# Performance work log

Hardware: AMD Instinct MI355X
Metric: run time of the kernel (lower is better)

The kernel has to match this reference:

```python
import jax, jax.numpy as jnp
import numpy as np

NUM_USERS = 600000
NUM_ITEMS = 400000
NUM_NODES = NUM_USERS + NUM_ITEMS
DIM = 64
NUM_EDGES = 8000000


def setup_inputs() -> dict:
    key = jax.random.key(0)
    k1, k2, k3, k4 = jax.random.split(key, 4)
    users_emb = jax.random.normal(k1, (NUM_USERS, DIM), dtype=jnp.float32)
    items_emb = jax.random.normal(k2, (NUM_ITEMS, DIM), dtype=jnp.float32)
    edge_index = jax.random.randint(k3, (2, NUM_EDGES), 0, NUM_NODES, dtype=jnp.int64)
    edge_values = jax.random.uniform(k4, (NUM_EDGES,), dtype=jnp.float32)
    return {
        "users_emb": users_emb,
        "items_emb": items_emb,
        "edge_index": edge_index,
        "edge_values": edge_values,
    }


def reference(users_emb, items_emb, edge_index, edge_values):
    # all_emb = cat([users_emb, items_emb])  -> [N, d]
    num_user = users_emb.shape[0]
    num_item = items_emb.shape[0]
    all_emb = jnp.concatenate([users_emb, items_emb], axis=0)
    # SpMM: out[r] = sum_{e: row[e]==r} val[e] * all_emb[col[e]]
    rows, cols = edge_index[0], edge_index[1]
    messages = all_emb[cols] * edge_values[:, None]  # [E, d] gather + scale
    out = jax.ops.segment_sum(messages, rows, num_segments=num_user + num_item)
    h_u2 = out[:num_user]
    h_i2 = out[num_user:]
    return (h_u2, h_i2)
```

## Files before the change

kernel.cpp:

```cpp
#include <hip/hip_runtime.h>

#define DIM 64
#define RPB 1024
#define RPB_SHIFT 10
#define NBMAX 1024
#define CHUNK 4096
#define EPT 16
#define CAPT 35
#define SREC_CAP (CAPT * 256)
#define NPGF 32

typedef unsigned long long u64;
typedef unsigned int u32;
typedef unsigned short u16;
typedef float f4v __attribute__((ext_vector_type(4)));
typedef _Float16 h4 __attribute__((ext_vector_type(4)));
typedef _Float16 h8 __attribute__((ext_vector_type(8)));

__global__ void detect_idx_width(const unsigned int* __restrict__ idx_words,
                                 int* __restrict__ flag) {
    __shared__ unsigned int s_or[256];
    unsigned int acc = 0;
    for (int i = threadIdx.x; i < 4096; i += blockDim.x)
        acc |= idx_words[2 * i + 1];
    s_or[threadIdx.x] = acc;
    __syncthreads();
    for (int s = 128; s > 0; s >>= 1) {
        if (threadIdx.x < s) s_or[threadIdx.x] |= s_or[threadIdx.x + s];
        __syncthreads();
    }
    if (threadIdx.x == 0) *flag = (s_or[0] == 0) ? 1 : 0;
}

__device__ __forceinline__ int load_idx(const void* ei, int use64, long long i) {
    return use64 ? (int)((const long long*)ei)[i] : ((const int*)ei)[i];
}

__device__ __forceinline__ int load_idx_nt(const void* ei, int use64, long long i) {
    return use64 ? (int)__builtin_nontemporal_load(&((const long long*)ei)[i])
                 : __builtin_nontemporal_load(&((const int*)ei)[i]);
}

__device__ __forceinline__ u32 quad_scan_ex(u32 qs, u32* wtot, int tid, u32* total_out) {
    u32 inc = qs;
    #pragma unroll
    for (int d = 1; d < 64; d <<= 1) {
        u32 v = __shfl_up(inc, d, 64);
        if ((tid & 63) >= d) inc += v;
    }
    if ((tid & 63) == 63) wtot[tid >> 6] = inc;
    __syncthreads();
    int w = tid >> 6;
    u32 woff = 0;
    #pragma unroll
    for (int k = 0; k < 3; ++k) woff += (k < w) ? wtot[k] : 0;
    if (total_out) *total_out = wtot[0] + wtot[1] + wtot[2] + wtot[3];
    return woff + inc - qs;
}

__global__ __launch_bounds__(256) void convert_emb(const f4v* __restrict__ u4,
                                                   const f4v* __restrict__ i4,
                                                   long long usz4, long long tot4,
                                                   h4* __restrict__ dst) {
    long long stride = (long long)gridDim.x * blockDim.x;
    for (long long idx = (long long)blockIdx.x * blockDim.x + threadIdx.x;
         idx < tot4; idx += stride) {
        const f4v* src = (idx < usz4) ? (u4 + idx) : (i4 + (idx - usz4));
        f4v f = __builtin_nontemporal_load(src);
        h4 o;
        o.x = (_Float16)f.x; o.y = (_Float16)f.y;
        o.z = (_Float16)f.z; o.w = (_Float16)f.w;
        dst[idx] = o;
    }
}

__global__ __launch_bounds__(256) void hist_coarse(const void* __restrict__ ei,
                                                   const int* __restrict__ flag,
                                                   int* __restrict__ counts,
                                                   int num_edges) {
    __shared__ int h[NBMAX];
    for (int b = threadIdx.x; b < NBMAX; b += 256) h[b] = 0;
    __syncthreads();
    int use64 = *flag;
    long long tid = (long long)blockIdx.x * 256 + threadIdx.x;
    long long stride = (long long)gridDim.x * 256;
    long long npairs = (long long)num_edges >> 1;
    const u64* p = (const u64*)ei;
    if (use64) {
        for (long long e = tid; e < npairs; e += stride) {
            u64 a = __builtin_nontemporal_load(&p[2 * e]);
            u64 b = __builtin_nontemporal_load(&p[2 * e + 1]);
            atomicAdd(&h[(int)(u32)a >> RPB_SHIFT], 1);
            atomicAdd(&h[(int)(u32)b >> RPB_SHIFT], 1);
        }
    } else {
        for (long long e = tid; e < npairs; e += stride) {
            u64 v = __builtin_nontemporal_load(&p[e]);
            atomicAdd(&h[(int)(u32)v >> RPB_SHIFT], 1);
            atomicAdd(&h[(int)(u32)(v >> 32) >> RPB_SHIFT], 1);
        }
    }
    if (tid == 0 && (num_edges & 1)) {
        int r = load_idx(ei, use64, num_edges - 1);
        atomicAdd(&h[r >> RPB_SHIFT], 1);
    }
    __syncthreads();
    for (int b = threadIdx.x; b < NBMAX; b += 256)
        if (h[b]) atomicAdd(&counts[b], h[b]);
}

__global__ __launch_bounds__(256) void scan_buckets(const int* __restrict__ counts,
                                                    int* __restrict__ offs,
                                                    int* __restrict__ gcursor,
                                                    int* __restrict__ offs2, int nbkt) {
    __shared__ u32 wtot[4];
    int t = threadIdx.x;
    int4 h = ((const int4*)counts)[t];
    u32 qs = (u32)(h.x + h.y + h.z + h.w);
    u32 total;
    u32 ex = quad_scan_ex(qs, wtot, t, &total);
    int o0 = (int)ex, o1 = o0 + h.x, o2 = o1 + h.y, o3 = o2 + h.z;
    offs[4*t] = o0; offs[4*t+1] = o1; offs[4*t+2] = o2; offs[4*t+3] = o3;
    gcursor[4*t] = o0; gcursor[4*t+1] = o1; gcursor[4*t+2] = o2; gcursor[4*t+3] = o3;
    if (t == 255) {
        offs[NBMAX] = (int)total;
        if (offs2) offs2[(long long)nbkt << RPB_SHIFT] = (int)total;
    }
}

__global__ __launch_bounds__(256) void bin_edges(const void* __restrict__ ei,
                                                 const float* __restrict__ vals,
                                                 const int* __restrict__ flag,
                                                 int* __restrict__ gcursor,
                                                 u64* __restrict__ recs,
                                                 int num_edges) {
    __shared__ u32 hist[NBMAX];
    __shared__ u32 scanL[NBMAX];
    __shared__ u32 gbase[NBMAX];
    __shared__ u32 wtot[4];
    __shared__ u64 payload[CHUNK];
    __shared__ u16 bidv[CHUNK];

    int tid = threadIdx.x;
    long long base = (long long)blockIdx.x * CHUNK;
    int n = (int)min((long long)CHUNK, (long long)num_edges - base);
    int use64 = *flag;

    for (int b = tid; b < NBMAX; b += 256) hist[b] = 0;
    __syncthreads();

    int rows_[EPT]; int cols_[EPT]; float ws_[EPT];
    #pragma unroll
    for (int i = 0; i < EPT; ++i) {
        int j = tid + i * 256;
        rows_[i] = -1;
        if (j < n) {
            long long e = base + j;
            rows_[i] = load_idx_nt(ei, use64, e);
            cols_[i] = load_idx_nt(ei, use64, (long long)num_edges + e);
            ws_[i]   = __builtin_nontemporal_load(&vals[e]);
            atomicAdd(&hist[rows_[i] >> RPB_SHIFT], 1u);
        }
    }
    __syncthreads();

    u32 h0 = hist[4*tid], h1 = hist[4*tid+1], h2 = hist[4*tid+2], h3 = hist[4*tid+3];
    u32 ex = quad_scan_ex(h0 + h1 + h2 + h3, wtot, tid, nullptr);
    scanL[4*tid]   = ex;
    scanL[4*tid+1] = ex + h0;
    scanL[4*tid+2] = ex + h0 + h1;
    scanL[4*tid+3] = ex + h0 + h1 + h2;
    __syncthreads();

    for (int b = tid; b < NBMAX; b += 256) {
        u32 c = hist[b];
        gbase[b] = c ? (u32)atomicAdd(&gcursor[b], (int)c) : 0u;
    }
    __syncthreads();
    for (int b = tid; b < NBMAX; b += 256) hist[b] = scanL[b];
    __syncthreads();

    #pragma unroll
    for (int i = 0; i < EPT; ++i) {
        if (rows_[i] >= 0) {
            int b = rows_[i] >> RPB_SHIFT;
            u32 pos = atomicAdd(&hist[b], 1u);
            u32 rl = (u32)(rows_[i] & (RPB - 1));
            payload[pos] = ((u64)__float_as_uint(ws_[i]) << 32) | (rl << 20) | (u32)cols_[i];
            bidv[pos] = (u16)b;
        }
    }
    __syncthreads();

    for (int j = tid; j < n; j += 256) {
        u64 rec = payload[j];
        int b = bidv[j];
        recs[gbase[b] + (u32)j - scanL[b]] = rec;
    }
}

#define ACC8(P0, P1, W, V) \
    P0.x += W * (float)V[0]; P0.y += W * (float)V[1]; \
    P0.z += W * (float)V[2]; P0.w += W * (float)V[3]; \
    P1.x += W * (float)V[4]; P1.y += W * (float)V[5]; \
    P1.z += W * (float)V[6]; P1.w += W * (float)V[7];

__global__ __launch_bounds__(256, 2) void sortgather_h(const int* __restrict__ offs,
                                                       const u64* __restrict__ recs,
                                                       const h8* __restrict__ hemb8,
                                                       float* __restrict__ out,
                                                       int num_nodes) {
    __shared__ u64 s_recs[SREC_CAP];
    __shared__ u32 node_beg[RPB + 1];
    __shared__ u32 cursor[RPB];
    __shared__ u32 wtot[4];

    int b  = blockIdx.x;
    int t  = threadIdx.x;
    int l8 = t & 7;
    int g  = t >> 3;
    int beg = offs[b], end = offs[b + 1];
    int cnt = end - beg;
    int row0 = b << RPB_SHIFT;

    if (cnt <= SREC_CAP) {
        u64 r_[CAPT];
        #pragma unroll
        for (int k = 0; k < CAPT; ++k) {
            int j = t + k * 256;
            r_[k] = (j < cnt) ? __builtin_nontemporal_load(&recs[beg + j]) : 0ull;
        }
        for (int i = t; i < RPB; i += 256) cursor[i] = 0;
        __syncthreads();
        #pragma unroll
        for (int k = 0; k < CAPT; ++k) {
            int j = t + k * 256;
            if (j < cnt) atomicAdd(&cursor[(u32)(r_[k] >> 20) & (RPB - 1)], 1u);
        }
        __syncthreads();
        u32 c0[4]; u32 s = 0;
        #pragma unroll
        for (int i = 0; i < 4; ++i) { c0[i] = cursor[t * 4 + i]; s += c0[i]; }
        u32 ex = quad_scan_ex(s, wtot, t, nullptr);
        #pragma unroll
        for (int i = 0; i < 4; ++i) {
            node_beg[t * 4 + i] = ex;
            cursor[t * 4 + i] = ex;
            ex += c0[i];
        }
        if (t == 0) node_beg[RPB] = (u32)cnt;
        __syncthreads();
        #pragma unroll
        for (int k = 0; k < CAPT; ++k) {
            int j = t + k * 256;
            if (j < cnt) {
                u32 rl = (u32)(r_[k] >> 20) & (RPB - 1);
                u32 pos = atomicAdd(&cursor[rl], 1u);
                s_recs[pos] = r_[k];
            }
        }
        __syncthreads();

        for (int nn = 0; nn < NPGF; ++nn) {
            int ln = g * NPGF + nn;
            int node = row0 + ln;
            if (node >= num_nodes) break;
            int nb = (int)node_beg[ln];
            int ne = (int)node_beg[ln + 1];

            float4 p0 = make_float4(0.f,0.f,0.f,0.f), p1 = make_float4(0.f,0.f,0.f,0.f);
            float4 q0 = make_float4(0.f,0.f,0.f,0.f), q1 = make_float4(0.f,0.f,0.f,0.f);

            int i = nb;
            for (; i + 8 <= ne; i += 8) {
                u64 s0 = s_recs[i];     u64 s1 = s_recs[i + 1];
                u64 s2 = s_recs[i + 2]; u64 s3 = s_recs[i + 3];
                u64 s4 = s_recs[i + 4]; u64 s5 = s_recs[i + 5];
                u64 s6 = s_recs[i + 6]; u64 s7 = s_recs[i + 7];
                h8 v0 = hemb8[(((u32)s0 & 0xFFFFFu) << 3) + l8];
                h8 v1 = hemb8[(((u32)s1 & 0xFFFFFu) << 3) + l8];
                h8 v2 = hemb8[(((u32)s2 & 0xFFFFFu) << 3) + l8];
                h8 v3 = hemb8[(((u32)s3 & 0xFFFFFu) << 3) + l8];
                h8 v4 = hemb8[(((u32)s4 & 0xFFFFFu) << 3) + l8];
                h8 v5 = hemb8[(((u32)s5 & 0xFFFFFu) << 3) + l8];
                h8 v6 = hemb8[(((u32)s6 & 0xFFFFFu) << 3) + l8];
                h8 v7 = hemb8[(((u32)s7 & 0xFFFFFu) << 3) + l8];
                float w0 = __uint_as_float((u32)(s0 >> 32));
                float w1 = __uint_as_float((u32)(s1 >> 32));
                float w2 = __uint_as_float((u32)(s2 >> 32));
                float w3 = __uint_as_float((u32)(s3 >> 32));
                float w4 = __uint_as_float((u32)(s4 >> 32));
                float w5 = __uint_as_float((u32)(s5 >> 32));
                float w6 = __uint_as_float((u32)(s6 >> 32));
                float w7 = __uint_as_float((u32)(s7 >> 32));
                ACC8(p0, p1, w0, v0); ACC8(q0, q1, w1, v1);
                ACC8(p0, p1, w2, v2); ACC8(q0, q1, w3, v3);
                ACC8(p0, p1, w4, v4); ACC8(q0, q1, w5, v5);
                ACC8(p0, p1, w6, v6); ACC8(q0, q1, w7, v7);
            }
            if (i < ne) {
                int last = ne - 1;
                int e1 = min(i + 1, last), e2 = min(i + 2, last);
                int e3 = min(i + 3, last), e4 = min(i + 4, last);
                int e5 = min(i + 5, last), e6 = min(i + 6, last);
                u64 s0 = s_recs[i];  u64 s1 = s_recs[e1];
                u64 s2 = s_recs[e2]; u64 s3 = s_recs[e3];
                u64 s4 = s_recs[e4]; u64 s5 = s_recs[e5];
                u64 s6 = s_recs[e6];
                h8 v0 = hemb8[(((u32)s0 & 0xFFFFFu) << 3) + l8];
                h8 v1 = hemb8[(((u32)s1 & 0xFFFFFu) << 3) + l8];
                h8 v2 = hemb8[(((u32)s2 & 0xFFFFFu) << 3) + l8];
                h8 v3 = hemb8[(((u32)s3 & 0xFFFFFu) << 3) + l8];
                h8 v4 = hemb8[(((u32)s4 & 0xFFFFFu) << 3) + l8];
                h8 v5 = hemb8[(((u32)s5 & 0xFFFFFu) << 3) + l8];
                h8 v6 = hemb8[(((u32)s6 & 0xFFFFFu) << 3) + l8];
                float w0 = __uint_as_float((u32)(s0 >> 32));
                float w1 = (i + 1 < ne) ? __uint_as_float((u32)(s1 >> 32)) : 0.f;
                float w2 = (i + 2 < ne) ? __uint_as_float((u32)(s2 >> 32)) : 0.f;
                float w3 = (i + 3 < ne) ? __uint_as_float((u32)(s3 >> 32)) : 0.f;
                float w4 = (i + 4 < ne) ? __uint_as_float((u32)(s4 >> 32)) : 0.f;
                float w5 = (i + 5 < ne) ? __uint_as_float((u32)(s5 >> 32)) : 0.f;
                float w6 = (i + 6 < ne) ? __uint_as_float((u32)(s6 >> 32)) : 0.f;
                ACC8(p0, p1, w0, v0); ACC8(q0, q1, w1, v1);
                ACC8(p0, p1, w2, v2); ACC8(q0, q1, w3, v3);
                ACC8(p0, p1, w4, v4); ACC8(q0, q1, w5, v5);
                ACC8(p0, p1, w6, v6);
            }

            p0.x += q0.x; p0.y += q0.y; p0.z += q0.z; p0.w += q0.w;
            p1.x += q1.x; p1.y += q1.y; p1.z += q1.z; p1.w += q1.w;
            f4v o0; o0.x = p0.x; o0.y = p0.y; o0.z = p0.z; o0.w = p0.w;
            f4v o1; o1.x = p1.x; o1.y = p1.y; o1.z = p1.z; o1.w = p1.w;
            f4v* dst = (f4v*)out + ((long long)node << 4) + (l8 << 1);
            __builtin_nontemporal_store(o0, dst);
            __builtin_nontemporal_store(o1, dst + 1);
        }
    } else {
        for (int nn = 0; nn < NPGF; ++nn) {
            int ln = g * NPGF + nn;
            int node = row0 + ln;
            if (node >= num_nodes) break;
            u32 rl = (u32)ln;

            float4 p0 = make_float4(0.f,0.f,0.f,0.f), p1 = make_float4(0.f,0.f,0.f,0.f);
            float4 q0 = make_float4(0.f,0.f,0.f,0.f), q1 = make_float4(0.f,0.f,0.f,0.f);
            int last = end - 1;
            u32 rm = RPB - 1;
            for (int i = beg; i < end; i += 4) {
                int e1 = min(i + 1, last), e2 = min(i + 2, last), e3 = min(i + 3, last);
                u64 s0 = recs[i];  u64 s1 = recs[e1];
                u64 s2 = recs[e2]; u64 s3 = recs[e3];
                h8 v0 = hemb8[(((u32)s0 & 0xFFFFFu) << 3) + l8];
                h8 v1 = hemb8[(((u32)s1 & 0xFFFFFu) << 3) + l8];
                h8 v2 = hemb8[(((u32)s2 & 0xFFFFFu) << 3) + l8];
                h8 v3 = hemb8[(((u32)s3 & 0xFFFFFu) << 3) + l8];
                float w0 = ((((u32)(s0 >> 20)) & rm) == rl)
                           ? __uint_as_float((u32)(s0 >> 32)) : 0.f;
                float w1 = (((((u32)(s1 >> 20)) & rm) == rl) & (i + 1 < end))
                           ? __uint_as_float((u32)(s1 >> 32)) : 0.f;
                float w2 = (((((u32)(s2 >> 20)) & rm) == rl) & (i + 2 < end))
                           ? __uint_as_float((u32)(s2 >> 32)) : 0.f;
                float w3 = (((((u32)(s3 >> 20)) & rm) == rl) & (i + 3 < end))
                           ? __uint_as_float((u32)(s3 >> 32)) : 0.f;
                ACC8(p0, p1, w0, v0); ACC8(q0, q1, w1, v1);
                ACC8(p0, p1, w2, v2); ACC8(q0, q1, w3, v3);
            }
            p0.x += q0.x; p0.y += q0.y; p0.z += q0.z; p0.w += q0.w;
            p1.x += q1.x; p1.y += q1.y; p1.z += q1.z; p1.w += q1.w;
            f4v o0; o0.x = p0.x; o0.y = p0.y; o0.z = p0.z; o0.w = p0.w;
            f4v o1; o1.x = p1.x; o1.y = p1.y; o1.z = p1.z; o1.w = p1.w;
            f4v* dst = (f4v*)out + ((long long)node << 4) + (l8 << 1);
            __builtin_nontemporal_store(o0, dst);
            __builtin_nontemporal_store(o1, dst + 1);
        }
    }
}

__global__ __launch_bounds__(256, 2) void sort_bucket(const int* __restrict__ offs,
                                                      u64* __restrict__ recs,
                                                      int* __restrict__ offs2) {
    __shared__ u32 bins[RPB];
    __shared__ u32 wtot[4];
    int b = blockIdx.x;
    int t = threadIdx.x;
    int beg = offs[b], end = offs[b + 1];
    int cnt = end - beg;
    int row0 = b << RPB_SHIFT;

    if (cnt > CAPT * 256) {
        for (int i = t; i < RPB; i += 256) offs2[row0 + i] = -(b + 1);
        return;
    }

    u64 r_[CAPT];
    #pragma unroll
    for (int k = 0; k < CAPT; ++k) {
        int j = t + k * 256;
        r_[k] = (j < cnt) ? recs[beg + j] : 0ull;
    }
    for (int i = t; i < RPB; i += 256) bins[i] = 0;
    __syncthreads();

    #pragma unroll
    for (int k = 0; k < CAPT; ++k) {
        int j = t + k * 256;
        if (j < cnt) atomicAdd(&bins[(u32)(r_[k] >> 20) & (RPB - 1)], 1u);
    }
    __syncthreads();

    u32 c0[4]; u32 s = 0;
    #pragma unroll
    for (int i = 0; i < 4; ++i) { c0[i] = bins[t * 4 + i]; s += c0[i]; }
    u32 ex = quad_scan_ex(s, wtot, t, nullptr);
    #pragma unroll
    for (int i = 0; i < 4; ++i) {
        bins[t * 4 + i] = ex;
        offs2[row0 + t * 4 + i] = beg + (int)ex;
        ex += c0[i];
    }
    __syncthreads();

    #pragma unroll
    for (int k = 0; k < CAPT; ++k) {
        int j = t + k * 256;
        if (j < cnt) {
            u32 rl = (u32)(r_[k] >> 20) & (RPB - 1);
            u32 pos = atomicAdd(&bins[rl], 1u);
            recs[beg + pos] = r_[k];
        }
    }
}

__device__ __forceinline__ void gstep(u64 s, u32 rl,
                                      const float* __restrict__ users,
                                      const float* __restrict__ items_m,
                                      int num_users, int l16, float4& a) {
    int c = (int)(s & 0xFFFFFu);
    float w = __uint_as_float((u32)(s >> 32));
    w = (((u32)(s >> 20) & (RPB - 1)) == rl) ? w : 0.f;
    const float* p = ((c < num_users) ? users : items_m) + ((u32)c << 6);
    float4 m = reinterpret_cast<const float4*>(p)[l16];
    a.x += w * m.x; a.y += w * m.y; a.z += w * m.z; a.w += w * m.w;
}

__global__ __launch_bounds__(256) void gather_nodes(const int* __restrict__ offs,
                                                    const int* __restrict__ offs2,
                                                    const u64* __restrict__ recs,
                                                    const float* __restrict__ users,
                                                    const float* __restrict__ items_m,
                                                    float* __restrict__ out,
                                                    int num_users, int num_nodes) {
    int node = blockIdx.x * (blockDim.x >> 6) + (threadIdx.x >> 6);
    int lane = threadIdx.x & 63;
    if (node >= num_nodes) return;
    int q   = lane >> 4;
    int l16 = lane & 15;

    int beg = offs2[node];
    int end = offs2[node + 1];
    if (beg < 0) { int b = node >> RPB_SHIFT; beg = offs[b]; end = offs[b + 1]; }
    else if (end < 0) { end = offs[(node >> RPB_SHIFT) + 1]; }
    u32 rl = (u32)(node & (RPB - 1));

    float4 a0 = make_float4(0.f, 0.f, 0.f, 0.f);
    float4 a1 = make_float4(0.f, 0.f, 0.f, 0.f);

    int i = beg + q;
    for (; i + 4 < end; i += 8) {
        u64 s0 = recs[i];
        u64 s1 = recs[i + 4];
        gstep(s0, rl, users, items_m, num_users, l16, a0);
        gstep(s1, rl, users, items_m, num_users, l16, a1);
    }
    if (i < end) {
        u64 s0 = recs[i];
        gstep(s0, rl, users, items_m, num_users, l16, a0);
    }
    a0.x += a1.x; a0.y += a1.y; a0.z += a1.z; a0.w += a1.w;

    for (int msk = 16; msk <= 32; msk <<= 1) {
        a0.x += __shfl_xor(a0.x, msk, 64);
        a0.y += __shfl_xor(a0.y, msk, 64);
        a0.z += __shfl_xor(a0.z, msk, 64);
        a0.w += __shfl_xor(a0.w, msk, 64);
    }
    if (q == 0)
        reinterpret_cast<float4*>(out)[(long long)node * 16 + l16] = a0;
}

__global__ __launch_bounds__(256) void scatter_edges(const void* __restrict__ edge_index,
                                                     const float* __restrict__ vals,
                                                     const float* __restrict__ users,
                                                     const float* __restrict__ items,
                                                     float* __restrict__ out,
                                                     const int* __restrict__ idx64_flag,
                                                     int num_users, int num_edges) {
    long long gid = (long long)blockIdx.x * blockDim.x + threadIdx.x;
    long long e = gid >> 4;
    int lane = (int)(gid & 15);
    if (e >= num_edges) return;
    int use64 = *idx64_flag;
    int r = load_idx(edge_index, use64, e);
    int c = load_idx(edge_index, use64, (long long)num_edges + e);
    float w = vals[e];
    const float* src = (c < num_users)
        ? (users + (long long)c * DIM)
        : (items + (long long)(c - num_users) * DIM);
    float4 m = reinterpret_cast<const float4*>(src)[lane];
    float* dst = out + (long long)r * DIM + lane * 4;
    unsafeAtomicAdd(dst + 0, m.x * w);
    unsafeAtomicAdd(dst + 1, m.y * w);
    unsafeAtomicAdd(dst + 2, m.z * w);
    unsafeAtomicAdd(dst + 3, m.w * w);
}

extern "C" void kernel_launch(void* const* d_in, const int* in_sizes, int n_in,
                              void* d_out, int out_size, void* d_ws, size_t ws_size,
                              hipStream_t stream) {
    const float* users = (const float*)d_in[0];
    const float* items = (const float*)d_in[1];
    const void*  eidx  = d_in[2];
    const float* vals  = (const float*)d_in[3];
    float* out = (float*)d_out;

    int num_users = in_sizes[0] / DIM;
    int num_items = in_sizes[1] / DIM;
    int num_nodes = num_users + num_items;
    int num_edges = in_sizes[3];
    int nbkt = (num_nodes + RPB - 1) >> RPB_SHIFT;

    size_t off = 0;
    auto alloc = [&](size_t bytes) { size_t p = off; off = (off + bytes + 255) & ~(size_t)255; return p; };
    size_t o_flag   = alloc(4);
    size_t o_counts = alloc((size_t)NBMAX * 4);
    size_t o_offs   = alloc(((size_t)NBMAX + 1) * 4);
    size_t o_gcur   = alloc((size_t)NBMAX * 4);
    size_t o_recs   = alloc((size_t)num_edges * 8 + 64);
    size_t o_offs2  = alloc((((size_t)nbkt << RPB_SHIFT) + 1) * 4);
    size_t need_base = off;
    size_t o_hemb   = alloc((size_t)num_nodes * DIM * 2);
    size_t need_f16 = off;

    char* ws = (char*)d_ws;
    int* flag = (int*)(ws + o_flag);

    detect_idx_width<<<1, 256, 0, stream>>>((const unsigned int*)eidx, flag);

    if (ws_size < need_base || nbkt > NBMAX || num_nodes > (1 << 20)) {
        hipMemsetAsync(d_out, 0, (size_t)out_size * sizeof(float), stream);
        long long total_threads = (long long)num_edges * 16;
        long long grid = (total_threads + 255) / 256;
        scatter_edges<<<(int)grid, 256, 0, stream>>>(
            eidx, vals, users, items, out, flag, num_users, num_edges);
        return;
    }

    int* counts  = (int*)(ws + o_counts);
    int* offs    = (int*)(ws + o_offs);
    int* gcursor = (int*)(ws + o_gcur);
    u64* recs    = (u64*)(ws + o_recs);
    int* offs2   = (int*)(ws + o_offs2);
    h4*  hemb4   = (h4*)(ws + o_hemb);

    bool use_f16 = (ws_size >= need_f16) && ((DIM % 8) == 0);

    hipMemsetAsync(counts, 0, (size_t)NBMAX * 4, stream);

    if (use_f16) {
        long long usz4 = (long long)num_users * DIM / 4;
        long long tot4 = (long long)num_nodes * DIM / 4;
        convert_emb<<<2048, 256, 0, stream>>>((const f4v*)users, (const f4v*)items,
                                              usz4, tot4, hemb4);
    }

    hist_coarse<<<768, 256, 0, stream>>>(eidx, flag, counts, num_edges);
    scan_buckets<<<1, 256, 0, stream>>>(counts, offs, gcursor,
                                        use_f16 ? nullptr : offs2, nbkt);

    int bin_grid = (num_edges + CHUNK - 1) / CHUNK;
    bin_edges<<<bin_grid, 256, 0, stream>>>(eidx, vals, flag, gcursor, recs, num_edges);

    if (use_f16) {
        sortgather_h<<<nbkt, 256, 0, stream>>>(offs, recs, (const h8*)hemb4,
                                               out, num_nodes);
    } else {
        sort_bucket<<<nbkt, 256, 0, stream>>>(offs, recs, offs2);
        int gg = (num_nodes + 3) / 4;
        const float* items_m = items - (size_t)num_users * DIM;
        gather_nodes<<<gg, 256, 0, stream>>>(offs, offs2, recs, users, items_m, out,
                                             num_users, num_nodes);
    }
}
```

Measured before the change: 399.6 us.

## Fuse embedding conversion with histogram, simplify edge binning to direct scatter

Merges the fp16 embedding conversion and the coarse row histogram into one launch with disjoint block roles, and moves the counts zeroing into the index-width detection kernel, dropping a memset and a launch. Binning now uses larger chunks with 512 threads, reads the rows twice and scatters records straight to global memory via per-bucket atomic cursors, with no shared-memory staging or local scan. This cuts launch overhead and shared-memory use, at the cost of rereading indices and making less coalesced global writes.

```diff
diff --git a/kernel.cpp b/kernel.cpp
--- a/kernel.cpp
+++ b/kernel.cpp
@@ -4,8 +4,7 @@
 #define RPB 1024
 #define RPB_SHIFT 10
 #define NBMAX 1024
-#define CHUNK 4096
-#define EPT 16
+#define BCHUNK 16384
 #define CAPT 35
 #define SREC_CAP (CAPT * 256)
 #define NPGF 32
@@ -18,8 +17,11 @@
 typedef _Float16 h8 __attribute__((ext_vector_type(8)));
 
 __global__ void detect_idx_width(const unsigned int* __restrict__ idx_words,
-                                 int* __restrict__ flag) {
+                                 int* __restrict__ flag,
+                                 int* __restrict__ counts) {
     __shared__ unsigned int s_or[256];
+    if (counts)
+        for (int i = threadIdx.x; i < NBMAX; i += 256) counts[i] = 0;
     unsigned int acc = 0;
     for (int i = threadIdx.x; i < 4096; i += blockDim.x)
         acc |= idx_words[2 * i + 1];
@@ -34,11 +36,6 @@
 
 __device__ __forceinline__ int load_idx(const void* ei, int use64, long long i) {
     return use64 ? (int)((const long long*)ei)[i] : ((const int*)ei)[i];
-}
-
-__device__ __forceinline__ int load_idx_nt(const void* ei, int use64, long long i) {
-    return use64 ? (int)__builtin_nontemporal_load(&((const long long*)ei)[i])
-                 : __builtin_nontemporal_load(&((const int*)ei)[i]);
 }
 
 __device__ __forceinline__ u32 quad_scan_ex(u32 qs, u32* wtot, int tid, u32* total_out) {
@@ -58,19 +55,57 @@
     return woff + inc - qs;
 }
 
-__global__ __launch_bounds__(256) void convert_emb(const f4v* __restrict__ u4,
-                                                   const f4v* __restrict__ i4,
-                                                   long long usz4, long long tot4,
-                                                   h4* __restrict__ dst) {
-    long long stride = (long long)gridDim.x * blockDim.x;
-    for (long long idx = (long long)blockIdx.x * blockDim.x + threadIdx.x;
-         idx < tot4; idx += stride) {
-        const f4v* src = (idx < usz4) ? (u4 + idx) : (i4 + (idx - usz4));
-        f4v f = __builtin_nontemporal_load(src);
-        h4 o;
-        o.x = (_Float16)f.x; o.y = (_Float16)f.y;
-        o.z = (_Float16)f.z; o.w = (_Float16)f.w;
-        dst[idx] = o;
+__global__ __launch_bounds__(256) void prep(const f4v* __restrict__ u4,
+                                            const f4v* __restrict__ i4,
+                                            long long usz4, long long tot4,
+                                            h4* __restrict__ dst,
+                                            const void* __restrict__ ei,
+                                            const int* __restrict__ flag,
+                                            int* __restrict__ counts,
+                                            int num_edges,
+                                            int convBlocks, int histBlocks) {
+    if ((int)blockIdx.x < convBlocks) {
+        long long stride = (long long)convBlocks * 256;
+        for (long long idx = (long long)blockIdx.x * 256 + threadIdx.x;
+             idx < tot4; idx += stride) {
+            const f4v* src = (idx < usz4) ? (u4 + idx) : (i4 + (idx - usz4));
+            f4v f = __builtin_nontemporal_load(src);
+            h4 o;
+            o.x = (_Float16)f.x; o.y = (_Float16)f.y;
+            o.z = (_Float16)f.z; o.w = (_Float16)f.w;
+            dst[idx] = o;
+        }
+    } else {
+        __shared__ int h[NBMAX];
+        for (int b = threadIdx.x; b < NBMAX; b += 256) h[b] = 0;
+        __syncthreads();
+        int use64 = *flag;
+        int hb = (int)blockIdx.x - convBlocks;
+        long long tid = (long long)hb * 256 + threadIdx.x;
+        long long stride = (long long)histBlocks * 256;
+        long long npairs = (long long)num_edges >> 1;
+        const u64* p = (const u64*)ei;
+        if (use64) {
+            for (long long e = tid; e < npairs; e += stride) {
+                u64 a = __builtin_nontemporal_load(&p[2 * e]);
+                u64 b = __builtin_nontemporal_load(&p[2 * e + 1]);
+                atomicAdd(&h[(int)(u32)a >> RPB_SHIFT], 1);
+                atomicAdd(&h[(int)(u32)b >> RPB_SHIFT], 1);
+            }
+        } else {
+            for (long long e = tid; e < npairs; e += stride) {
+                u64 v = __builtin_nontemporal_load(&p[e]);
+                atomicAdd(&h[(int)(u32)v >> RPB_SHIFT], 1);
+                atomicAdd(&h[(int)(u32)(v >> 32) >> RPB_SHIFT], 1);
+            }
+        }
+        if (tid == 0 && (num_edges & 1)) {
+            int r = load_idx(ei, use64, num_edges - 1);
+            atomicAdd(&h[r >> RPB_SHIFT], 1);
+        }
+        __syncthreads();
+        for (int b = threadIdx.x; b < NBMAX; b += 256)
+            if (h[b]) atomicAdd(&counts[b], h[b]);
     }
 }
 
@@ -128,74 +163,46 @@
     }
 }
 
-__global__ __launch_bounds__(256) void bin_edges(const void* __restrict__ ei,
-                                                 const float* __restrict__ vals,
-                                                 const int* __restrict__ flag,
-                                                 int* __restrict__ gcursor,
-                                                 u64* __restrict__ recs,
-                                                 int num_edges) {
+__global__ __launch_bounds__(512) void bin_edges2(const void* __restrict__ ei,
+                                                  const float* __restrict__ vals,
+                                                  const int* __restrict__ flag,
+                                                  int* __restrict__ gcursor,
+                                                  u64* __restrict__ recs,
+                                                  int num_edges) {
     __shared__ u32 hist[NBMAX];
-    __shared__ u32 scanL[NBMAX];
     __shared__ u32 gbase[NBMAX];
-    __shared__ u32 wtot[4];
-    __shared__ u64 payload[CHUNK];
-    __shared__ u16 bidv[CHUNK];
-
     int tid = threadIdx.x;
-    long long base = (long long)blockIdx.x * CHUNK;
-    int n = (int)min((long long)CHUNK, (long long)num_edges - base);
+    long long base = (long long)blockIdx.x * BCHUNK;
+    int n = (int)min((long long)BCHUNK, (long long)num_edges - base);
     int use64 = *flag;
 
-    for (int b = tid; b < NBMAX; b += 256) hist[b] = 0;
-    __syncthreads();
-
-    int rows_[EPT]; int cols_[EPT]; float ws_[EPT];
-    #pragma unroll
-    for (int i = 0; i < EPT; ++i) {
-        int j = tid + i * 256;
-        rows_[i] = -1;
-        if (j < n) {
-            long long e = base + j;
-            rows_[i] = load_idx_nt(ei, use64, e);
-            cols_[i] = load_idx_nt(ei, use64, (long long)num_edges + e);
-            ws_[i]   = __builtin_nontemporal_load(&vals[e]);
-            atomicAdd(&hist[rows_[i] >> RPB_SHIFT], 1u);
-        }
-    }
-    __syncthreads();
-
-    u32 h0 = hist[4*tid], h1 = hist[4*tid+1], h2 = hist[4*tid+2], h3 = hist[4*tid+3];
-    u32 ex = quad_scan_ex(h0 + h1 + h2 + h3, wtot, tid, nullptr);
-    scanL[4*tid]   = ex;
-    scanL[4*tid+1] = ex + h0;
-    scanL[4*tid+2] = ex + h0 + h1;
-    scanL[4*tid+3] = ex + h0 + h1 + h2;
-    __syncthreads();
-
-    for (int b = tid; b < NBMAX; b += 256) {
+    for (int b = tid; b < NBMAX; b += 512) hist[b] = 0;
+    __syncthreads();
+
+    for (int j = tid; j < n; j += 512) {
+        int r = load_idx(ei, use64, base + j);
+        atomicAdd(&hist[r >> RPB_SHIFT], 1u);
+    }
+    __syncthreads();
+
+    for (int b = tid; b < NBMAX; b += 512) {
         u32 c = hist[b];
         gbase[b] = c ? (u32)atomicAdd(&gcursor[b], (int)c) : 0u;
     }
     __syncthreads();
-    for (int b = tid; b < NBMAX; b += 256) hist[b] = scanL[b];
-    __syncthreads();
-
-    #pragma unroll
-    for (int i = 0; i < EPT; ++i) {
-        if (rows_[i] >= 0) {
-            int b = rows_[i] >> RPB_SHIFT;
-            u32 pos = atomicAdd(&hist[b], 1u);
-            u32 rl = (u32)(rows_[i] & (RPB - 1));
-            payload[pos] = ((u64)__float_as_uint(ws_[i]) << 32) | (rl << 20) | (u32)cols_[i];
-            bidv[pos] = (u16)b;
-        }
-    }
-    __syncthreads();
-
-    for (int j = tid; j < n; j += 256) {
-        u64 rec = payload[j];
-        int b = bidv[j];
-        recs[gbase[b] + (u32)j - scanL[b]] = rec;
+    for (int b = tid; b < NBMAX; b += 512) hist[b] = 0;
+    __syncthreads();
+
+    for (int j = tid; j < n; j += 512) {
+        long long e = base + j;
+        int r = load_idx(ei, use64, e);
+        int c = load_idx(ei, use64, (long long)num_edges + e);
+        float w = vals[e];
+        int b = r >> RPB_SHIFT;
+        u32 pos = gbase[b] + atomicAdd(&hist[b], 1u);
+        u64 rec = ((u64)__float_as_uint(w) << 32)
+                | ((u32)(r & (RPB - 1)) << 20) | (u32)c;
+        recs[pos] = rec;
     }
 }
 
@@ -544,9 +551,8 @@
     char* ws = (char*)d_ws;
     int* flag = (int*)(ws + o_flag);
 
-    detect_idx_width<<<1, 256, 0, stream>>>((const unsigned int*)eidx, flag);
-
     if (ws_size < need_base || nbkt > NBMAX || num_nodes > (1 << 20)) {
+        detect_idx_width<<<1, 256, 0, stream>>>((const unsigned int*)eidx, flag, nullptr);
         hipMemsetAsync(d_out, 0, (size_t)out_size * sizeof(float), stream);
         long long total_threads = (long long)num_edges * 16;
         long long grid = (total_threads + 255) / 256;
@@ -564,21 +570,26 @@
 
     bool use_f16 = (ws_size >= need_f16) && ((DIM % 8) == 0);
 
-    hipMemsetAsync(counts, 0, (size_t)NBMAX * 4, stream);
+    detect_idx_width<<<1, 256, 0, stream>>>((const unsigned int*)eidx, flag, counts);
+
+    long long usz4 = (long long)num_users * DIM / 4;
+    long long tot4 = (long long)num_nodes * DIM / 4;
 
     if (use_f16) {
-        long long usz4 = (long long)num_users * DIM / 4;
-        long long tot4 = (long long)num_nodes * DIM / 4;
-        convert_emb<<<2048, 256, 0, stream>>>((const f4v*)users, (const f4v*)items,
-                                              usz4, tot4, hemb4);
-    }
-
-    hist_coarse<<<768, 256, 0, stream>>>(eidx, flag, counts, num_edges);
+        const int convB = 2048, histB = 768;
+        prep<<<convB + histB, 256, 0, stream>>>((const f4v*)users, (const f4v*)items,
+                                                usz4, tot4, hemb4,
+                                                eidx, flag, counts, num_edges,
+                                                convB, histB);
+    } else {
+        hist_coarse<<<768, 256, 0, stream>>>(eidx, flag, counts, num_edges);
+    }
+
     scan_buckets<<<1, 256, 0, stream>>>(counts, offs, gcursor,
                                         use_f16 ? nullptr : offs2, nbkt);
 
-    int bin_grid = (num_edges + CHUNK - 1) / CHUNK;
-    bin_edges<<<bin_grid, 256, 0, stream>>>(eidx, vals, flag, gcursor, recs, num_edges);
+    int bin_grid = (num_edges + BCHUNK - 1) / BCHUNK;
+    bin_edges2<<<bin_grid, 512, 0, stream>>>(eidx, vals, flag, gcursor, recs, num_edges);
 
     if (use_f16) {
         sortgather_h<<<nbkt, 256, 0, stream>>>(offs, recs, (const h8*)hemb4,
```

Measured after the change: 460.1 us. 15.1% more time.
